# Kernel tuning notes

Hardware: AMD Instinct MI355X
Metric: run time of the kernel (lower is better)

Reference implementation:

```python
import jax, jax.numpy as jnp
import numpy as np

BIG = 1e8  # replaces inf entries in the cost matrix, as in the torch module


def _hungarian(cost):
    """Min-cost bipartite assignment for an (n, m) cost matrix with n <= m.
    Returns, for each row i, the assigned column (same optimum as
    scipy.optimize.linear_sum_assignment; rows come back in sorted order).
    Classic O(n*m^2) shortest-augmenting-path algorithm with potentials."""
    n, m = cost.shape
    INF = np.inf
    u = np.zeros(n + 1)
    v = np.zeros(m + 1)
    p = np.zeros(m + 1, dtype=np.int64)   # p[j]: row matched to col j (1-based; 0 = free)
    way = np.zeros(m + 1, dtype=np.int64)
    for i in range(1, n + 1):
        p[0] = i
        j0 = 0
        minv = np.full(m + 1, INF)
        used = np.zeros(m + 1, dtype=bool)
        while True:
            used[j0] = True
            i0 = p[j0]
            cur = cost[i0 - 1, :] - u[i0] - v[1:]
            free = ~used[1:]
            better = free & (cur < minv[1:])
            minv[1:] = np.where(better, cur, minv[1:])
            way[1:] = np.where(better, j0, way[1:])
            cand = np.where(free, minv[1:], INF)
            j1 = int(np.argmin(cand)) + 1
            delta = cand[j1 - 1]
            u[p[used]] += delta
            v[used] -= delta
            minv[~used] -= delta
            j0 = j1
            if p[j0] == 0:
                break
        while j0 != 0:
            j1 = int(way[j0])
            p[j0] = p[j1]
            j0 = j1
    ans = np.zeros(n, dtype=np.int64)
    for j in range(1, m + 1):
        if p[j] != 0:
            ans[p[j] - 1] = j - 1
    return ans


def _matched_labels(outputs, gold, weight):
    """Per-sample Hungarian matching on the restricted-softmax NLL cost,
    exactly as the torch module: cost[b] = -log_softmax(outputs[b][:, gold[b]], 1) * w[gold[b]].
    Matching is detached (host-side), mirroring scipy linear_sum_assignment."""
    B, S, C = outputs.shape
    idx = jnp.broadcast_to(gold[:, None, :], (B, S, S))
    sub = jnp.take_along_axis(outputs, idx, axis=2)                  # [B,S,S] logits at gold cols
    cost = -jax.nn.log_softmax(sub, axis=2) * weight[gold][:, None, :]
    cost = jnp.where(jnp.isinf(cost), BIG, cost)
    cost_np = np.asarray(cost, dtype=np.float64)
    gold_np = np.asarray(gold)
    match = np.empty_like(gold_np)
    for b in range(B):
        col = _hungarian(cost_np[b])                                 # row i -> gold column
        match[b] = gold_np[b][col]
    return jnp.asarray(match)


def setup_inputs() -> dict:
    key = jax.random.key(0)
    k1, k2 = jax.random.split(key)
    B, S, C = 128, 20, 32000
    outputs = jax.random.normal(k1, (B, S, C), dtype=jnp.float32)
    gold_label_ids = jax.random.randint(k2, (B, S), 0, C)
    mask = jnp.ones((B, S), dtype=bool)
    weight = jnp.ones((C,), dtype=jnp.float32)
    return {"outputs": outputs, "gold_label_ids": gold_label_ids, "mask": mask, "weight": weight}


def reference(outputs, gold_label_ids, mask, weight):
    eps = 1e-8
    match = _matched_labels(outputs, gold_label_ids, weight)         # [B,S] matched class ids
    logp = jax.nn.log_softmax(outputs, axis=-1)                      # [B,S,C]
    nll = -jnp.take_along_axis(logp, match[..., None], axis=2)[..., 0] * weight[match]
    m = mask.reshape(-1).astype(outputs.dtype)
    loss = nll.reshape(-1) * m
    return jnp.sum(loss) / (jnp.sum(m) + eps)
```

## Files before the change

### kernel.cpp

```cpp
#include <hip/hip_runtime.h>
#include <hip/hip_bf16.h>
#include <math.h>

#define NB 128
#define NS 20
#define NC 32000
#define RPB 2
#define NLSE (NB * NS / RPB)
#define NBLOCKS (NB + NLSE)

static __device__ __forceinline__ float fmin_x1(float x) {
    int t = __builtin_amdgcn_update_dpp(0, __float_as_int(x), 0xB1, 0xf, 0xf, true);
    return fminf(x, __int_as_float(t));
}
static __device__ __forceinline__ float fmin_x2(float x) {
    int t = __builtin_amdgcn_update_dpp(0, __float_as_int(x), 0x4E, 0xf, 0xf, true);
    return fminf(x, __int_as_float(t));
}
static __device__ __forceinline__ float fmin_x4(float x) {
    int t = __builtin_amdgcn_ds_swizzle(__float_as_int(x), 0x101F);
    return fminf(x, __int_as_float(t));
}
static __device__ __forceinline__ float fmin_x8(float x) {
    int t = __builtin_amdgcn_ds_swizzle(__float_as_int(x), 0x201F);
    return fminf(x, __int_as_float(t));
}
static __device__ __forceinline__ float fmin_x16(float x) {
    int t = __builtin_amdgcn_ds_swizzle(__float_as_int(x), 0x401F);
    return fminf(x, __int_as_float(t));
}
static __device__ __forceinline__ float readlane_f(float x, int lane) {
    return __int_as_float(__builtin_amdgcn_readlane(__float_as_int(x), lane));
}

__global__ __launch_bounds__(256) void mega_kernel(
        const float* __restrict__ outputs,
        const int* __restrict__ gold,
        const float* __restrict__ weight,
        int* __restrict__ match_col,
        float* __restrict__ sub_ws,
        float* __restrict__ logZ) {

    if (blockIdx.x < NB) {
        const int b = blockIdx.x;
        const int* g = gold + b * NS;
        __shared__ float cst[NS * NS];
        __shared__ float lzs[NS];

        for (int e = threadIdx.x; e < NS * NS; e += 256) {
            int i = e / NS, j = e - i * NS;
            float x = outputs[(size_t)(b * NS + i) * NC + g[j]];
            cst[e] = x;
            sub_ws[(size_t)(b * NS + i) * NS + j] = x;
        }
        __syncthreads();
        if (threadIdx.x < NS) {
            int i = threadIdx.x;
            float mx = cst[i * NS];
#pragma unroll
            for (int j = 1; j < NS; ++j) mx = fmaxf(mx, cst[i * NS + j]);
            float s = 0.f;
#pragma unroll
            for (int j = 0; j < NS; ++j) s += __expf(cst[i * NS + j] - mx);
            lzs[i] = mx + __logf(s);
        }
        __syncthreads();
        for (int e = threadIdx.x; e < NS * NS; e += 256) {
            int i = e / NS, j = e - i * NS;
            float c = -(cst[e] - lzs[i]) * weight[g[j]];
            if (isinf(c)) c = 1e8f;
            cst[e] = c;
        }
        __syncthreads();
        if (threadIdx.x >= 64) return;

        const int lane = threadIdx.x;
        const float FINF = INFINITY;
        float up_j = 0.f, v_j = 0.f;
        int p_j = 0, way_j = 0;
        const bool is_col = (lane >= 1 && lane <= NS);

        for (int i = 1; i <= NS; ++i) {
            if (lane == 0) { p_j = i; up_j = 0.f; }
            int j0 = 0;
            float minv_j = FINF;
            bool used_j = false;
            while (true) {
                int pp = __builtin_amdgcn_readlane(p_j, j0);
                if (pp == 0) break;
                if (lane == j0) used_j = true;
                float upp = readlane_f(up_j, j0);
                float cv = cst[is_col ? (pp - 1) * NS + (lane - 1) : 0];
                if (is_col && !used_j) {
                    float cur = cv - upp - v_j;
                    if (cur < minv_j) { minv_j = cur; way_j = j0; }
                }
                float cand = (is_col && !used_j) ? minv_j : FINF;
                float mval = fmin_x16(fmin_x8(fmin_x4(fmin_x2(fmin_x1(cand)))));
                unsigned long long bal = __ballot(cand == mval) & 0xFFFFFFFFull;
                int j1 = __ffsll(bal) - 1;
                float delta = mval;
                if (used_j) { up_j += delta; v_j -= delta; }
                else if (is_col) minv_j -= delta;
                j0 = j1;
            }
            while (j0 != 0) {
                int   j1   = __builtin_amdgcn_readlane(way_j, j0);
                int   pj1  = __builtin_amdgcn_readlane(p_j, j1);
                float upj1 = readlane_f(up_j, j1);
                if (lane == j0) { p_j = pj1; up_j = upj1; }
                j0 = j1;
            }
        }
        if (is_col && p_j != 0) {
            match_col[b * NS + (p_j - 1)] = lane - 1;
        }
    } else {
        __shared__ float smx[4], ssm[4];
        const int rbase = (blockIdx.x - NB) * RPB;
        for (int rr = 0; rr < RPB; ++rr) {
            const int row = rbase + rr;
            const float4* rp = (const float4*)(outputs + (size_t)row * NC);
            const int n4 = NC / 4;
            const int nfull = (n4 / 1024) * 1024;

            float m = -INFINITY;
            float s = 0.f;
            for (int base = 0; base < nfull; base += 1024) {
                int i0 = base + threadIdx.x;
                float4 a = rp[i0];
                float4 bq = rp[i0 + 256];
                float4 c = rp[i0 + 512];
                float4 d = rp[i0 + 768];
                float m4 = fmaxf(fmaxf(fmaxf(a.x, a.y), fmaxf(a.z, a.w)),
                                 fmaxf(fmaxf(bq.x, bq.y), fmaxf(bq.z, bq.w)));
                m4 = fmaxf(m4, fmaxf(fmaxf(fmaxf(c.x, c.y), fmaxf(c.z, c.w)),
                                     fmaxf(fmaxf(d.x, d.y), fmaxf(d.z, d.w))));
                float nm = fmaxf(m, m4);
                float sl = __expf(a.x - nm) + __expf(a.y - nm)
                         + __expf(a.z - nm) + __expf(a.w - nm);
                sl += __expf(bq.x - nm) + __expf(bq.y - nm)
                    + __expf(bq.z - nm) + __expf(bq.w - nm);
                sl += __expf(c.x - nm) + __expf(c.y - nm)
                    + __expf(c.z - nm) + __expf(c.w - nm);
                sl += __expf(d.x - nm) + __expf(d.y - nm)
                    + __expf(d.z - nm) + __expf(d.w - nm);
                s = s * __expf(m - nm) + sl;
                m = nm;
            }
            for (int idx = nfull + threadIdx.x; idx < n4; idx += 256) {
                float4 x = rp[idx];
                float m4 = fmaxf(fmaxf(x.x, x.y), fmaxf(x.z, x.w));
                float nm = fmaxf(m, m4);
                s = s * __expf(m - nm)
                  + __expf(x.x - nm) + __expf(x.y - nm)
                  + __expf(x.z - nm) + __expf(x.w - nm);
                m = nm;
            }
            for (int off = 1; off < 64; off <<= 1) {
                float om = __shfl_xor(m, off);
                float os = __shfl_xor(s, off);
                float nm = fmaxf(m, om);
                s = s * __expf(m - nm) + os * __expf(om - nm);
                m = nm;
            }
            __syncthreads();
            int wid = threadIdx.x >> 6;
            if ((threadIdx.x & 63) == 0) { smx[wid] = m; ssm[wid] = s; }
            __syncthreads();
            if (threadIdx.x == 0) {
                float M = smx[0], S = ssm[0];
                for (int w = 1; w < 4; ++w) {
                    float om = smx[w], os = ssm[w];
                    float nm = fmaxf(M, om);
                    S = S * __expf(M - nm) + os * __expf(om - nm);
                    M = nm;
                }
                logZ[row] = M + __logf(S);
            }
        }
    }
}

__global__ __launch_bounds__(256) void final_kernel(
        const int* __restrict__ match_col,
        const float* __restrict__ sub_ws,
        const float* __restrict__ logZ,
        const float* __restrict__ weight,
        const int* __restrict__ gold,
        const unsigned char* __restrict__ mask,
        float* __restrict__ out) {
    double nsum = 0.0, msum = 0.0;
    for (int r = threadIdx.x; r < NB * NS; r += 256) {
        int b = r / NS;
        int col = match_col[r];
        float x = sub_ws[(size_t)r * NS + col];
        float w = weight[gold[b * NS + col]];
        float nll = -(x - logZ[r]) * w;
        float mk = mask[r] ? 1.f : 0.f;
        nsum += (double)(nll * mk);
        msum += (double)mk;
    }
    for (int off = 1; off < 64; off <<= 1) {
        nsum += __shfl_xor(nsum, off);
        msum += __shfl_xor(msum, off);
    }
    __shared__ double sn[4], sm[4];
    int wid = threadIdx.x >> 6;
    if ((threadIdx.x & 63) == 0) { sn[wid] = nsum; sm[wid] = msum; }
    __syncthreads();
    if (threadIdx.x == 0) {
        double N = 0.0, M = 0.0;
        for (int w = 0; w < 4; ++w) { N += sn[w]; M += sm[w]; }
        out[0] = (float)(N / (M + 1e-8));
    }
}

extern "C" void kernel_launch(void* const* d_in, const int* in_sizes, int n_in,
                              void* d_out, int out_size, void* d_ws, size_t ws_size,
                              hipStream_t stream) {
    const float* outputs        = (const float*)d_in[0];
    const int*   gold           = (const int*)d_in[1];
    const unsigned char* mask   = (const unsigned char*)d_in[2];
    const float* weight         = (const float*)d_in[3];
    float* out = (float*)d_out;

    char* ws = (char*)d_ws;
    int*   match_col = (int*)ws;
    float* logZ      = (float*)(ws + (size_t)NB * NS * 4);
    float* sub_ws    = (float*)(ws + (size_t)NB * NS * 8);

    mega_kernel<<<NBLOCKS, 256, 0, stream>>>(outputs, gold, weight,
                                             match_col, sub_ws, logZ);
    final_kernel<<<1, 256, 0, stream>>>(match_col, sub_ws, logZ, weight, gold,
                                        mask, out);
}
```

Measured before the change: 69.76 us.

## Rebalance LSE rows so Hungarian blocks also compute logZ after matching

The grid shrinks from 1408 to 1280 blocks. The 128 Hungarian blocks, once matching is done, each compute one logsumexp row. Blocks 128-255 take three rows each and the rest take two. This is meant to put idle lanes in the long-running matching blocks to work and cut the number of separate block waves. The final reduction kernel is widened to 512 threads. The risk is that the matching blocks' extra row lengthens the critical path, and that three-row blocks become the new tail.

New measurement: 69.08 us. No clear change (-1.0%).

```diff
diff --git a/kernel.cpp b/kernel.cpp
--- a/kernel.cpp
+++ b/kernel.cpp
@@ -5,9 +5,8 @@
 #define NB 128
 #define NS 20
 #define NC 32000
-#define RPB 2
-#define NLSE (NB * NS / RPB)
-#define NBLOCKS (NB + NLSE)
+#define NROWS (NB * NS)
+#define NBLOCKS 1280
 
 static __device__ __forceinline__ float fmin_x1(float x) {
     int t = __builtin_amdgcn_update_dpp(0, __float_as_int(x), 0xB1, 0xf, 0xf, true);
@@ -41,8 +40,11 @@
         float* __restrict__ sub_ws,
         float* __restrict__ logZ) {
 
-    if (blockIdx.x < NB) {
-        const int b = blockIdx.x;
+    __shared__ float smx[4], ssm[4];
+    const int bid = blockIdx.x;
+
+    if (bid < NB) {
+        const int b = bid;
         const int* g = gold + b * NS;
         __shared__ float cst[NS * NS];
         __shared__ float lzs[NS];
@@ -72,117 +74,122 @@
             cst[e] = c;
         }
         __syncthreads();
-        if (threadIdx.x >= 64) return;
-
-        const int lane = threadIdx.x;
-        const float FINF = INFINITY;
-        float up_j = 0.f, v_j = 0.f;
-        int p_j = 0, way_j = 0;
-        const bool is_col = (lane >= 1 && lane <= NS);
-
-        for (int i = 1; i <= NS; ++i) {
-            if (lane == 0) { p_j = i; up_j = 0.f; }
-            int j0 = 0;
-            float minv_j = FINF;
-            bool used_j = false;
-            while (true) {
-                int pp = __builtin_amdgcn_readlane(p_j, j0);
-                if (pp == 0) break;
-                if (lane == j0) used_j = true;
-                float upp = readlane_f(up_j, j0);
-                float cv = cst[is_col ? (pp - 1) * NS + (lane - 1) : 0];
-                if (is_col && !used_j) {
-                    float cur = cv - upp - v_j;
-                    if (cur < minv_j) { minv_j = cur; way_j = j0; }
+
+        if (threadIdx.x < 64) {
+            const int lane = threadIdx.x;
+            const float FINF = INFINITY;
+            float up_j = 0.f, v_j = 0.f;
+            int p_j = 0, way_j = 0;
+            const bool is_col = (lane >= 1 && lane <= NS);
+
+            for (int i = 1; i <= NS; ++i) {
+                if (lane == 0) { p_j = i; up_j = 0.f; }
+                int j0 = 0;
+                float minv_j = FINF;
+                bool used_j = false;
+                while (true) {
+                    int pp = __builtin_amdgcn_readlane(p_j, j0);
+                    if (pp == 0) break;
+                    if (lane == j0) used_j = true;
+                    float upp = readlane_f(up_j, j0);
+                    float cv = cst[is_col ? (pp - 1) * NS + (lane - 1) : 0];
+                    if (is_col && !used_j) {
+                        float curv = cv - upp - v_j;
+                        if (curv < minv_j) { minv_j = curv; way_j = j0; }
+                    }
+                    float cand = (is_col && !used_j) ? minv_j : FINF;
+                    float mval = fmin_x16(fmin_x8(fmin_x4(fmin_x2(fmin_x1(cand)))));
+                    unsigned long long bal = __ballot(cand == mval) & 0xFFFFFFFFull;
+                    int j1 = __ffsll(bal) - 1;
+                    float delta = mval;
+                    if (used_j) { up_j += delta; v_j -= delta; }
+                    else if (is_col) minv_j -= delta;
+                    j0 = j1;
                 }
-                float cand = (is_col && !used_j) ? minv_j : FINF;
-                float mval = fmin_x16(fmin_x8(fmin_x4(fmin_x2(fmin_x1(cand)))));
-                unsigned long long bal = __ballot(cand == mval) & 0xFFFFFFFFull;
-                int j1 = __ffsll(bal) - 1;
-                float delta = mval;
-                if (used_j) { up_j += delta; v_j -= delta; }
-                else if (is_col) minv_j -= delta;
-                j0 = j1;
+                while (j0 != 0) {
+                    int   j1   = __builtin_amdgcn_readlane(way_j, j0);
+                    int   pj1  = __builtin_amdgcn_readlane(p_j, j1);
+                    float upj1 = readlane_f(up_j, j1);
+                    if (lane == j0) { p_j = pj1; up_j = upj1; }
+                    j0 = j1;
+                }
             }
-            while (j0 != 0) {
-                int   j1   = __builtin_amdgcn_readlane(way_j, j0);
-                int   pj1  = __builtin_amdgcn_readlane(p_j, j1);
-                float upj1 = readlane_f(up_j, j1);
-                if (lane == j0) { p_j = pj1; up_j = upj1; }
-                j0 = j1;
+            if (is_col && p_j != 0) {
+                match_col[b * NS + (p_j - 1)] = lane - 1;
             }
         }
-        if (is_col && p_j != 0) {
-            match_col[b * NS + (p_j - 1)] = lane - 1;
-        }
-    } else {
-        __shared__ float smx[4], ssm[4];
-        const int rbase = (blockIdx.x - NB) * RPB;
-        for (int rr = 0; rr < RPB; ++rr) {
-            const int row = rbase + rr;
-            const float4* rp = (const float4*)(outputs + (size_t)row * NC);
-            const int n4 = NC / 4;
-            const int nfull = (n4 / 1024) * 1024;
-
-            float m = -INFINITY;
-            float s = 0.f;
-            for (int base = 0; base < nfull; base += 1024) {
-                int i0 = base + threadIdx.x;
-                float4 a = rp[i0];
-                float4 bq = rp[i0 + 256];
-                float4 c = rp[i0 + 512];
-                float4 d = rp[i0 + 768];
-                float m4 = fmaxf(fmaxf(fmaxf(a.x, a.y), fmaxf(a.z, a.w)),
-                                 fmaxf(fmaxf(bq.x, bq.y), fmaxf(bq.z, bq.w)));
-                m4 = fmaxf(m4, fmaxf(fmaxf(fmaxf(c.x, c.y), fmaxf(c.z, c.w)),
-                                     fmaxf(fmaxf(d.x, d.y), fmaxf(d.z, d.w))));
-                float nm = fmaxf(m, m4);
-                float sl = __expf(a.x - nm) + __expf(a.y - nm)
-                         + __expf(a.z - nm) + __expf(a.w - nm);
-                sl += __expf(bq.x - nm) + __expf(bq.y - nm)
-                    + __expf(bq.z - nm) + __expf(bq.w - nm);
-                sl += __expf(c.x - nm) + __expf(c.y - nm)
-                    + __expf(c.z - nm) + __expf(c.w - nm);
-                sl += __expf(d.x - nm) + __expf(d.y - nm)
-                    + __expf(d.z - nm) + __expf(d.w - nm);
-                s = s * __expf(m - nm) + sl;
-                m = nm;
+        __syncthreads();
+    }
+
+    int r0, nr;
+    if (bid < 128)      { r0 = 2432 + bid;          nr = 1; }
+    else if (bid < 256) { r0 = (bid - 128) * 3;     nr = 3; }
+    else                { r0 = 384 + (bid - 256) * 2; nr = 2; }
+
+    for (int rr = 0; rr < nr; ++rr) {
+        const int row = r0 + rr;
+        const float4* rp = (const float4*)(outputs + (size_t)row * NC);
+        const int n4 = NC / 4;
+        const int nfull = (n4 / 1024) * 1024;
+
+        float m = -INFINITY;
+        float s = 0.f;
+        for (int base = 0; base < nfull; base += 1024) {
+            int i0 = base + threadIdx.x;
+            float4 a = rp[i0];
+            float4 bq = rp[i0 + 256];
+            float4 c = rp[i0 + 512];
+            float4 d = rp[i0 + 768];
+            float m4 = fmaxf(fmaxf(fmaxf(a.x, a.y), fmaxf(a.z, a.w)),
+                             fmaxf(fmaxf(bq.x, bq.y), fmaxf(bq.z, bq.w)));
+            m4 = fmaxf(m4, fmaxf(fmaxf(fmaxf(c.x, c.y), fmaxf(c.z, c.w)),
+                                 fmaxf(fmaxf(d.x, d.y), fmaxf(d.z, d.w))));
+            float nm = fmaxf(m, m4);
+            float sl = __expf(a.x - nm) + __expf(a.y - nm)
+                     + __expf(a.z - nm) + __expf(a.w - nm);
+            sl += __expf(bq.x - nm) + __expf(bq.y - nm)
+                + __expf(bq.z - nm) + __expf(bq.w - nm);
+            sl += __expf(c.x - nm) + __expf(c.y - nm)
+                + __expf(c.z - nm) + __expf(c.w - nm);
+            sl += __expf(d.x - nm) + __expf(d.y - nm)
+                + __expf(d.z - nm) + __expf(d.w - nm);
+            s = s * __expf(m - nm) + sl;
+            m = nm;
+        }
+        for (int idx = nfull + threadIdx.x; idx < n4; idx += 256) {
+            float4 x = rp[idx];
+            float m4 = fmaxf(fmaxf(x.x, x.y), fmaxf(x.z, x.w));
+            float nm = fmaxf(m, m4);
+            s = s * __expf(m - nm)
+              + __expf(x.x - nm) + __expf(x.y - nm)
+              + __expf(x.z - nm) + __expf(x.w - nm);
+            m = nm;
+        }
+        for (int off = 1; off < 64; off <<= 1) {
+            float om = __shfl_xor(m, off);
+            float os = __shfl_xor(s, off);
+            float nm = fmaxf(m, om);
+            s = s * __expf(m - nm) + os * __expf(om - nm);
+            m = nm;
+        }
+        __syncthreads();
+        int wid = threadIdx.x >> 6;
+        if ((threadIdx.x & 63) == 0) { smx[wid] = m; ssm[wid] = s; }
+        __syncthreads();
+        if (threadIdx.x == 0) {
+            float M = smx[0], S = ssm[0];
+            for (int w = 1; w < 4; ++w) {
+                float om = smx[w], os = ssm[w];
+                float nm = fmaxf(M, om);
+                S = S * __expf(M - nm) + os * __expf(om - nm);
+                M = nm;
             }
-            for (int idx = nfull + threadIdx.x; idx < n4; idx += 256) {
-                float4 x = rp[idx];
-                float m4 = fmaxf(fmaxf(x.x, x.y), fmaxf(x.z, x.w));
-                float nm = fmaxf(m, m4);
-                s = s * __expf(m - nm)
-                  + __expf(x.x - nm) + __expf(x.y - nm)
-                  + __expf(x.z - nm) + __expf(x.w - nm);
-                m = nm;
-            }
-            for (int off = 1; off < 64; off <<= 1) {
-                float om = __shfl_xor(m, off);
-                float os = __shfl_xor(s, off);
-                float nm = fmaxf(m, om);
-                s = s * __expf(m - nm) + os * __expf(om - nm);
-                m = nm;
-            }
-            __syncthreads();
-            int wid = threadIdx.x >> 6;
-            if ((threadIdx.x & 63) == 0) { smx[wid] = m; ssm[wid] = s; }
-            __syncthreads();
-            if (threadIdx.x == 0) {
-                float M = smx[0], S = ssm[0];
-                for (int w = 1; w < 4; ++w) {
-                    float om = smx[w], os = ssm[w];
-                    float nm = fmaxf(M, om);
-                    S = S * __expf(M - nm) + os * __expf(om - nm);
-                    M = nm;
-                }
-                logZ[row] = M + __logf(S);
-            }
-        }
-    }
-}
-
-__global__ __launch_bounds__(256) void final_kernel(
+            logZ[row] = M + __logf(S);
+        }
+    }
+}
+
+__global__ __launch_bounds__(512) void final_kernel(
         const int* __restrict__ match_col,
         const float* __restrict__ sub_ws,
         const float* __restrict__ logZ,
@@ -191,7 +198,7 @@
         const unsigned char* __restrict__ mask,
         float* __restrict__ out) {
     double nsum = 0.0, msum = 0.0;
-    for (int r = threadIdx.x; r < NB * NS; r += 256) {
+    for (int r = threadIdx.x; r < NROWS; r += 512) {
         int b = r / NS;
         int col = match_col[r];
         float x = sub_ws[(size_t)r * NS + col];
@@ -205,13 +212,13 @@
         nsum += __shfl_xor(nsum, off);
         msum += __shfl_xor(msum, off);
     }
-    __shared__ double sn[4], sm[4];
+    __shared__ double sn[8], sm[8];
     int wid = threadIdx.x >> 6;
     if ((threadIdx.x & 63) == 0) { sn[wid] = nsum; sm[wid] = msum; }
     __syncthreads();
     if (threadIdx.x == 0) {
         double N = 0.0, M = 0.0;
-        for (int w = 0; w < 4; ++w) { N += sn[w]; M += sm[w]; }
+        for (int w = 0; w < 8; ++w) { N += sn[w]; M += sm[w]; }
         out[0] = (float)(N / (M + 1e-8));
     }
 }
@@ -227,11 +234,11 @@
 
     char* ws = (char*)d_ws;
     int*   match_col = (int*)ws;
-    float* logZ      = (float*)(ws + (size_t)NB * NS * 4);
-    float* sub_ws    = (float*)(ws + (size_t)NB * NS * 8);
+    float* logZ      = (float*)(ws + (size_t)NROWS * 4);
+    float* sub_ws    = (float*)(ws + (size_t)NROWS * 8);
 
     mega_kernel<<<NBLOCKS, 256, 0, stream>>>(outputs, gold, weight,
                                              match_col, sub_ws, logZ);
-    final_kernel<<<1, 256, 0, stream>>>(match_col, sub_ws, logZ, weight, gold,
+    final_kernel<<<1, 512, 0, stream>>>(match_col, sub_ws, logZ, weight, gold,
                                         mask, out);
 }
```
